# Kernel optimization log

Measured on AMD Instinct MI355X. Metric: run time of the kernel, lower is better.

## Reference

```python
import jax, jax.numpy as jnp
import numpy as np

B, T, E, H, O = 64, 512, 512, 512, 512

def setup_inputs() -> dict:
    key = jax.random.key(0)
    k1, k2, k3, k4, k5 = jax.random.split(key, 5)
    s1 = 1.0 / np.sqrt(E + H)
    s2 = 1.0 / np.sqrt(H)
    return {
        "x": jax.random.normal(k1, (B, T, E), dtype=jnp.float32),
        "W1": jax.random.uniform(k2, (H, E + H), dtype=jnp.float32, minval=-s1, maxval=s1),
        "b1": jax.random.uniform(k3, (H,), dtype=jnp.float32, minval=-s1, maxval=s1),
        "W2": jax.random.uniform(k4, (O, H), dtype=jnp.float32, minval=-s2, maxval=s2),
        "b2": jax.random.uniform(k5, (O,), dtype=jnp.float32, minval=-s2, maxval=s2),
    }

def reference(x, W1, b1, W2, b2):
    b = x.shape[0]
    h0 = jnp.zeros((b, x.shape[2]), dtype=x.dtype)

    def step(hidden, xt):
        inp = jnp.concatenate([xt, hidden], axis=1)          # [b, e+h]
        hidden = jax.nn.relu(inp @ W1.T + b1)                # [b, h]
        out = hidden @ W2.T + b2                             # [b, o]
        return hidden, out

    # scan over time: x -> [t, b, e]
    h_final, outs = jax.lax.scan(step, h0, jnp.swapaxes(x, 0, 1))
    return jnp.swapaxes(outs, 0, 1), h_final
```

## Files before the change

### kernel.cpp

```cpp
#include <hip/hip_runtime.h>
#include <cstddef>

#define T_STEPS 512
#define BATCH   64
#define EDIM    512
#define HDIM    512
#define ODIM    512

#define HPAD    520
#define HALF    256

typedef __bf16 bf16;
typedef __bf16 bf16x4 __attribute__((ext_vector_type(4)));
typedef __bf16 bf16x8 __attribute__((ext_vector_type(8)));
typedef float  f32x4  __attribute__((ext_vector_type(4)));

template <typename XT, bool REMAP>
__global__ __launch_bounds__(256) void gemm_mfma_kernel(
    const XT* __restrict__ X, int ldx,
    const float* __restrict__ W, int ldw, int kw0,
    const float* __restrict__ bias,
    float* __restrict__ C, int ldc, int K)
{
  __shared__ __align__(16) bf16 Asm[8 * 64 * 8];
  __shared__ __align__(16) bf16 Bsm[8 * 64 * 8];

  const int tid  = threadIdx.x;
  const int row0 = blockIdx.x * 128;
  const int col0 = blockIdx.y * 128;
  const int w    = tid >> 6, lane = tid & 63;
  const int q    = lane >> 4, nl = lane & 15;
  const int wm   = w >> 1, wn = w & 1;

  f32x4 acc[4][4] = {};

  for (int k0 = 0; k0 < K; k0 += 32) {
#pragma unroll
    for (int rep = 0; rep < 2; ++rep) {
      int idx = tid + rep * 256;
      int mt = idx >> 6, l2 = idx & 63;
      const XT* src = X + (size_t)(row0 + mt * 16 + (l2 & 15)) * ldx
                        + k0 + (l2 >> 4) * 8;
      bf16x8 v;
#pragma unroll
      for (int u = 0; u < 8; ++u) v[u] = (bf16)(float)src[u];
      *(bf16x8*)&Asm[(size_t)idx * 8] = v;
    }
#pragma unroll
    for (int rep = 0; rep < 2; ++rep) {
      int idx = tid + rep * 256;
      int nt = idx >> 6, l2 = idx & 63;
      const float* src = W + (size_t)(col0 + nt * 16 + (l2 & 15)) * ldw
                           + kw0 + k0 + (l2 >> 4) * 8;
      bf16x8 v;
#pragma unroll
      for (int u = 0; u < 8; ++u) v[u] = (bf16)src[u];
      *(bf16x8*)&Bsm[(size_t)idx * 8] = v;
    }
    __syncthreads();

    bf16x8 a[4], b[4];
#pragma unroll
    for (int i = 0; i < 4; ++i)
      a[i] = *(bf16x8*)&Asm[(size_t)((wm * 4 + i) * 64 + lane) * 8];
#pragma unroll
    for (int j = 0; j < 4; ++j)
      b[j] = *(bf16x8*)&Bsm[(size_t)((wn * 4 + j) * 64 + lane) * 8];
#pragma unroll
    for (int i = 0; i < 4; ++i)
#pragma unroll
      for (int j = 0; j < 4; ++j)
        acc[i][j] = __builtin_amdgcn_mfma_f32_16x16x32_bf16(a[i], b[j], acc[i][j], 0, 0, 0);
    __syncthreads();
  }

#pragma unroll
  for (int i = 0; i < 4; ++i)
#pragma unroll
    for (int j = 0; j < 4; ++j) {
      int colg = col0 + wn * 64 + j * 16 + nl;
#pragma unroll
      for (int r = 0; r < 4; ++r) {
        size_t rowg = (size_t)(row0 + wm * 64 + i * 16 + q * 4 + r);
        size_t crow = REMAP ? (((rowg & (T_STEPS - 1)) << 6) | (rowg >> 9)) : rowg;
        C[crow * ldc + colg] = acc[i][j][r] + bias[colg];
      }
    }
}

__global__ __launch_bounds__(512, 2) void scan_split_kernel(
    const float* __restrict__ A,
    const float* __restrict__ W1,
    bf16* __restrict__ Hbf,
    int* __restrict__ flags)
{
  const int bid = blockIdx.x;
  int c, s;
  if (bid < 4)                   { c = bid;     s = 0; }
  else if (bid >= 8 && bid < 12) { c = bid - 8; s = 1; }
  else return;

  __shared__ __align__(16) bf16 hsm[16 * HPAD];

  const int tid   = threadIdx.x;
  const int col0  = s * HALF;
  const int pcol0 = (1 - s) * HALF;
  const int rb0   = c * 16;
  const int w     = tid >> 6, lane = tid & 63;
  const int q     = lane >> 4, nl = lane & 15;
  const int n0    = col0 + w * 32;
  const int m_ex  = tid >> 5;
  const int j_ex  = tid & 31;

  int* myflag = flags + (c * 2 + s) * 32;
  int* paflag = flags + (c * 2 + (1 - s)) * 32;

  bf16x8 Wreg[2][16];
#pragma unroll
  for (int i = 0; i < 2; ++i) {
    const float* wrow = W1 + (size_t)(n0 + i * 16 + nl) * (EDIM + HDIM) + EDIM + q * 8;
#pragma unroll
    for (int j = 0; j < 16; ++j) {
      int kg = (j < 8) ? (s * 8 + j) : ((1 - s) * 8 + (j - 8));
      const float* src = wrow + kg * 32;
      bf16x8 v;
#pragma unroll
      for (int u = 0; u < 8; ++u) v[u] = (bf16)src[u];
      Wreg[i][j] = v;
    }
  }

  f32x4 An[2];
  {
    const float* ap = A + ((size_t)(rb0 + nl)) * HDIM + n0 + q * 4;
    An[0] = *(const f32x4*)ap;
    An[1] = *(const f32x4*)(ap + 16);
  }

  f32x4 acc[2];

  for (int t = 0; t < T_STEPS; ++t) {
    acc[0] = An[0];
    acc[1] = An[1];
    {
      int tn = (t + 1 < T_STEPS) ? t + 1 : 0;
      const float* ap = A + ((size_t)tn * BATCH + rb0 + nl) * HDIM + n0 + q * 4;
      An[0] = *(const f32x4*)ap;
      An[1] = *(const f32x4*)(ap + 16);
    }

    unsigned long long p0 = 0, p1 = 0;
    if (t > 0) {
      while (__hip_atomic_load(paflag, __ATOMIC_RELAXED,
                               __HIP_MEMORY_SCOPE_AGENT) < t) {}
      unsigned long long* src = (unsigned long long*)(
          Hbf + ((size_t)(rb0 + m_ex) * T_STEPS + (t - 1)) * HDIM + pcol0 + j_ex * 8);
      p0 = __hip_atomic_load(src,     __ATOMIC_RELAXED, __HIP_MEMORY_SCOPE_AGENT);
      p1 = __hip_atomic_load(src + 1, __ATOMIC_RELAXED, __HIP_MEMORY_SCOPE_AGENT);
    }

    if (t > 0) {
#pragma unroll
      for (int kk = 0; kk < 8; ++kk) {
        bf16x8 af = *(bf16x8*)&hsm[nl * HPAD + col0 + kk * 32 + q * 8];
        acc[0] = __builtin_amdgcn_mfma_f32_16x16x32_bf16(Wreg[0][kk], af, acc[0], 0, 0, 0);
        acc[1] = __builtin_amdgcn_mfma_f32_16x16x32_bf16(Wreg[1][kk], af, acc[1], 0, 0, 0);
      }
      {
        union { unsigned long long u[2]; bf16x8 v; } P;
        P.u[0] = p0; P.u[1] = p1;
        *(bf16x8*)&hsm[m_ex * HPAD + pcol0 + j_ex * 8] = P.v;
      }
      __syncthreads();
#pragma unroll
      for (int kk = 0; kk < 8; ++kk) {
        bf16x8 af = *(bf16x8*)&hsm[nl * HPAD + pcol0 + kk * 32 + q * 8];
        acc[0] = __builtin_amdgcn_mfma_f32_16x16x32_bf16(Wreg[0][8 + kk], af, acc[0], 0, 0, 0);
        acc[1] = __builtin_amdgcn_mfma_f32_16x16x32_bf16(Wreg[1][8 + kk], af, acc[1], 0, 0, 0);
      }
    }

#pragma unroll
    for (int i = 0; i < 2; ++i) {
      bf16x4 hv;
#pragma unroll
      for (int r = 0; r < 4; ++r) hv[r] = (bf16)fmaxf(acc[i][r], 0.0f);
      *(bf16x4*)&hsm[nl * HPAD + n0 + i * 16 + q * 4] = hv;
      *(bf16x4*)(Hbf + ((size_t)(rb0 + nl) * T_STEPS + t) * HDIM + n0 + i * 16 + q * 4) = hv;
    }

    __syncthreads();
    if (tid == 0) {
      __threadfence();
      __hip_atomic_fetch_add(myflag, 1, __ATOMIC_RELAXED,
                             __HIP_MEMORY_SCOPE_AGENT);
    }
  }
}

__global__ __launch_bounds__(256) void copy_hfinal_kernel(
    const bf16* __restrict__ Hbf, float* __restrict__ out)
{
  int i = blockIdx.x * blockDim.x + threadIdx.x;
  int b = i / HDIM, n = i % HDIM;
  out[i] = (float)Hbf[((size_t)b * T_STEPS + (T_STEPS - 1)) * HDIM + n];
}

extern "C" void kernel_launch(void* const* d_in, const int* in_sizes, int n_in,
                              void* d_out, int out_size, void* d_ws, size_t ws_size,
                              hipStream_t stream) {
  const float* x  = (const float*)d_in[0];
  const float* W1 = (const float*)d_in[1];
  const float* b1 = (const float*)d_in[2];
  const float* W2 = (const float*)d_in[3];
  const float* b2 = (const float*)d_in[4];

  float* out = (float*)d_out;
  float* A   = out;

  bf16* Hbf  = (bf16*)d_ws;
  int* flags = (int*)((char*)d_ws + (size_t)BATCH * T_STEPS * HDIM * 2);

  hipMemsetAsync(flags, 0, 8 * 32 * sizeof(int), stream);

  {
    dim3 grid(BATCH * T_STEPS / 128, HDIM / 128);
    gemm_mfma_kernel<float, true><<<grid, 256, 0, stream>>>(
        x, EDIM, W1, EDIM + HDIM, 0, b1, A, HDIM, EDIM);
  }

  scan_split_kernel<<<16, 512, 0, stream>>>(A, W1, Hbf, flags);

  {
    dim3 grid(BATCH * T_STEPS / 128, ODIM / 128);
    gemm_mfma_kernel<bf16, false><<<grid, 256, 0, stream>>>(
        Hbf, HDIM, W2, HDIM, 0, b2, out, ODIM, HDIM);
  }

  copy_hfinal_kernel<<<(BATCH * HDIM) / 256, 256, 0, stream>>>(
      Hbf, out + (size_t)BATCH * T_STEPS * ODIM);
}
```

Measured before the change: 1.574 ms.

## Run recurrent scan in one block per batch chunk, dropping cross-block flag sync

The recurrent scan now gives each 16-row batch chunk a single 512-thread block that computes all 512 hidden columns, rather than two blocks that swapped half-states through global memory and spin-waited on atomic flags every timestep. Because the full recurrent weight slice no longer fits in registers, a quarter of it is staged in LDS (about 128 KB of dynamic shared memory) and the rest stays in registers. The hidden-state write to global memory is deferred by one step so it overlaps with the next step's compute. This removes the per-step inter-block handshake latency, but each block now does twice the MFMA work per step and reads part of the weights from LDS.

```diff
diff --git a/kernel.cpp b/kernel.cpp
--- a/kernel.cpp
+++ b/kernel.cpp
@@ -8,7 +8,9 @@
 #define ODIM    512
 
 #define HPAD    520
-#define HALF    256
+#define W_ELEMS (32 * 4 * 64 * 8)
+#define H_ELEMS (16 * HPAD)
+#define SMEM_BYTES ((W_ELEMS + H_ELEMS) * 2)
 
 typedef __bf16 bf16;
 typedef __bf16 bf16x4 __attribute__((ext_vector_type(4)));
@@ -88,113 +90,125 @@
     }
 }
 
-__global__ __launch_bounds__(512, 2) void scan_split_kernel(
+__global__ __launch_bounds__(512, 2) void scan_big_kernel(
     const float* __restrict__ A,
     const float* __restrict__ W1,
-    bf16* __restrict__ Hbf,
-    int* __restrict__ flags)
+    bf16* __restrict__ Hbf)
 {
-  const int bid = blockIdx.x;
-  int c, s;
-  if (bid < 4)                   { c = bid;     s = 0; }
-  else if (bid >= 8 && bid < 12) { c = bid - 8; s = 1; }
-  else return;
-
-  __shared__ __align__(16) bf16 hsm[16 * HPAD];
-
-  const int tid   = threadIdx.x;
-  const int col0  = s * HALF;
-  const int pcol0 = (1 - s) * HALF;
-  const int rb0   = c * 16;
-  const int w     = tid >> 6, lane = tid & 63;
-  const int q     = lane >> 4, nl = lane & 15;
-  const int n0    = col0 + w * 32;
-  const int m_ex  = tid >> 5;
-  const int j_ex  = tid & 31;
-
-  int* myflag = flags + (c * 2 + s) * 32;
-  int* paflag = flags + (c * 2 + (1 - s)) * 32;
-
-  bf16x8 Wreg[2][16];
-#pragma unroll
-  for (int i = 0; i < 2; ++i) {
-    const float* wrow = W1 + (size_t)(n0 + i * 16 + nl) * (EDIM + HDIM) + EDIM + q * 8;
-#pragma unroll
-    for (int j = 0; j < 16; ++j) {
-      int kg = (j < 8) ? (s * 8 + j) : ((1 - s) * 8 + (j - 8));
-      const float* src = wrow + kg * 32;
+  extern __shared__ __align__(16) bf16 smem[];
+  bf16* Wlds = smem;
+  bf16* hsm  = smem + W_ELEMS;
+
+  const int tid  = threadIdx.x;
+  const int c    = blockIdx.x;
+  const int w    = tid >> 6, lane = tid & 63;
+  const int q    = lane >> 4, nl = lane & 15;
+  const int rb0  = c * 16;
+
+  for (int idx = tid; idx < 32 * 4 * 64; idx += 512) {
+    int l  = idx & 63;
+    int kt = (idx >> 6) & 3;
+    int tg = idx >> 8;
+    int n  = tg * 16 + (l & 15);
+    int k  = kt * 32 + (l >> 4) * 8;
+    const float* src = W1 + (size_t)n * (EDIM + HDIM) + EDIM + k;
+    bf16x8 v;
+#pragma unroll
+    for (int u = 0; u < 8; ++u) v[u] = (bf16)src[u];
+    *(bf16x8*)&Wlds[(size_t)idx * 8] = v;
+  }
+
+  bf16x8 Wreg[4][12];
+#pragma unroll
+  for (int i = 0; i < 4; ++i) {
+    int n = w * 64 + i * 16 + nl;
+    const float* wrow = W1 + (size_t)n * (EDIM + HDIM) + EDIM;
+#pragma unroll
+    for (int kt2 = 0; kt2 < 12; ++kt2) {
+      const float* src = wrow + (kt2 + 4) * 32 + q * 8;
       bf16x8 v;
 #pragma unroll
       for (int u = 0; u < 8; ++u) v[u] = (bf16)src[u];
-      Wreg[i][j] = v;
-    }
-  }
-
-  f32x4 An[2];
-  {
-    const float* ap = A + ((size_t)(rb0 + nl)) * HDIM + n0 + q * 4;
-    An[0] = *(const f32x4*)ap;
+      Wreg[i][kt2] = v;
+    }
+  }
+  __syncthreads();
+
+  f32x4 An[4];
+  {
+    const float* ap = A + (size_t)(rb0 + nl) * HDIM + w * 64 + q * 4;
+    An[0] = *(const f32x4*)(ap);
     An[1] = *(const f32x4*)(ap + 16);
-  }
-
-  f32x4 acc[2];
+    An[2] = *(const f32x4*)(ap + 32);
+    An[3] = *(const f32x4*)(ap + 48);
+  }
+
+  f32x4  acc[4];
+  bf16x4 hprev[4];
 
   for (int t = 0; t < T_STEPS; ++t) {
-    acc[0] = An[0];
-    acc[1] = An[1];
+    if (t > 0) {
+      bf16* dst = Hbf + ((size_t)(rb0 + nl) * T_STEPS + (t - 1)) * HDIM
+                  + w * 64 + q * 4;
+      *(bf16x4*)(dst)      = hprev[0];
+      *(bf16x4*)(dst + 16) = hprev[1];
+      *(bf16x4*)(dst + 32) = hprev[2];
+      *(bf16x4*)(dst + 48) = hprev[3];
+    }
+
+#pragma unroll
+    for (int i = 0; i < 4; ++i) acc[i] = An[i];
     {
       int tn = (t + 1 < T_STEPS) ? t + 1 : 0;
-      const float* ap = A + ((size_t)tn * BATCH + rb0 + nl) * HDIM + n0 + q * 4;
-      An[0] = *(const f32x4*)ap;
+      const float* ap = A + ((size_t)tn * BATCH + rb0 + nl) * HDIM + w * 64 + q * 4;
+      An[0] = *(const f32x4*)(ap);
       An[1] = *(const f32x4*)(ap + 16);
-    }
-
-    unsigned long long p0 = 0, p1 = 0;
+      An[2] = *(const f32x4*)(ap + 32);
+      An[3] = *(const f32x4*)(ap + 48);
+    }
+
     if (t > 0) {
-      while (__hip_atomic_load(paflag, __ATOMIC_RELAXED,
-                               __HIP_MEMORY_SCOPE_AGENT) < t) {}
-      unsigned long long* src = (unsigned long long*)(
-          Hbf + ((size_t)(rb0 + m_ex) * T_STEPS + (t - 1)) * HDIM + pcol0 + j_ex * 8);
-      p0 = __hip_atomic_load(src,     __ATOMIC_RELAXED, __HIP_MEMORY_SCOPE_AGENT);
-      p1 = __hip_atomic_load(src + 1, __ATOMIC_RELAXED, __HIP_MEMORY_SCOPE_AGENT);
-    }
-
-    if (t > 0) {
-#pragma unroll
-      for (int kk = 0; kk < 8; ++kk) {
-        bf16x8 af = *(bf16x8*)&hsm[nl * HPAD + col0 + kk * 32 + q * 8];
-        acc[0] = __builtin_amdgcn_mfma_f32_16x16x32_bf16(Wreg[0][kk], af, acc[0], 0, 0, 0);
-        acc[1] = __builtin_amdgcn_mfma_f32_16x16x32_bf16(Wreg[1][kk], af, acc[1], 0, 0, 0);
+#pragma unroll
+      for (int kt = 0; kt < 16; ++kt) {
+        bf16x8 af = *(bf16x8*)&hsm[nl * HPAD + kt * 32 + q * 8];
+        if (kt < 4) {
+#pragma unroll
+          for (int i = 0; i < 4; ++i) {
+            bf16x8 wb = *(bf16x8*)&Wlds[(size_t)(((w * 4 + i) * 4 + kt) * 64 + lane) * 8];
+            acc[i] = __builtin_amdgcn_mfma_f32_16x16x32_bf16(wb, af, acc[i], 0, 0, 0);
+          }
+        } else {
+#pragma unroll
+          for (int i = 0; i < 4; ++i)
+            acc[i] = __builtin_amdgcn_mfma_f32_16x16x32_bf16(Wreg[i][kt - 4], af, acc[i], 0, 0, 0);
+        }
       }
-      {
-        union { unsigned long long u[2]; bf16x8 v; } P;
-        P.u[0] = p0; P.u[1] = p1;
-        *(bf16x8*)&hsm[m_ex * HPAD + pcol0 + j_ex * 8] = P.v;
+    }
+
+    __syncthreads();
+
+#pragma unroll
+    for (int i = 0; i < 4; ++i) {
+      bf16x4 hv;
+#pragma unroll
+      for (int r = 0; r < 4; ++r) {
+        float v = acc[i][r] > 0.0f ? acc[i][r] : 0.0f;
+        hv[r] = (bf16)v;
       }
-      __syncthreads();
-#pragma unroll
-      for (int kk = 0; kk < 8; ++kk) {
-        bf16x8 af = *(bf16x8*)&hsm[nl * HPAD + pcol0 + kk * 32 + q * 8];
-        acc[0] = __builtin_amdgcn_mfma_f32_16x16x32_bf16(Wreg[0][8 + kk], af, acc[0], 0, 0, 0);
-        acc[1] = __builtin_amdgcn_mfma_f32_16x16x32_bf16(Wreg[1][8 + kk], af, acc[1], 0, 0, 0);
-      }
-    }
-
-#pragma unroll
-    for (int i = 0; i < 2; ++i) {
-      bf16x4 hv;
-#pragma unroll
-      for (int r = 0; r < 4; ++r) hv[r] = (bf16)fmaxf(acc[i][r], 0.0f);
-      *(bf16x4*)&hsm[nl * HPAD + n0 + i * 16 + q * 4] = hv;
-      *(bf16x4*)(Hbf + ((size_t)(rb0 + nl) * T_STEPS + t) * HDIM + n0 + i * 16 + q * 4) = hv;
-    }
-
-    __syncthreads();
-    if (tid == 0) {
-      __threadfence();
-      __hip_atomic_fetch_add(myflag, 1, __ATOMIC_RELAXED,
-                             __HIP_MEMORY_SCOPE_AGENT);
-    }
+      *(bf16x4*)&hsm[nl * HPAD + w * 64 + i * 16 + q * 4] = hv;
+      hprev[i] = hv;
+    }
+
+    __syncthreads();
+  }
+
+  {
+    bf16* dst = Hbf + ((size_t)(rb0 + nl) * T_STEPS + (T_STEPS - 1)) * HDIM
+                + w * 64 + q * 4;
+    *(bf16x4*)(dst)      = hprev[0];
+    *(bf16x4*)(dst + 16) = hprev[1];
+    *(bf16x4*)(dst + 32) = hprev[2];
+    *(bf16x4*)(dst + 48) = hprev[3];
   }
 }
 
@@ -219,9 +233,6 @@
   float* A   = out;
 
   bf16* Hbf  = (bf16*)d_ws;
-  int* flags = (int*)((char*)d_ws + (size_t)BATCH * T_STEPS * HDIM * 2);
-
-  hipMemsetAsync(flags, 0, 8 * 32 * sizeof(int), stream);
 
   {
     dim3 grid(BATCH * T_STEPS / 128, HDIM / 128);
@@ -229,7 +240,10 @@
         x, EDIM, W1, EDIM + HDIM, 0, b1, A, HDIM, EDIM);
   }
 
-  scan_split_kernel<<<16, 512, 0, stream>>>(A, W1, Hbf, flags);
+  hipFuncSetAttribute(
+      reinterpret_cast<const void*>(scan_big_kernel),
+      hipFuncAttributeMaxDynamicSharedMemorySize, SMEM_BYTES);
+  scan_big_kernel<<<4, 512, SMEM_BYTES, stream>>>(A, W1, Hbf);
 
   {
     dim3 grid(BATCH * T_STEPS / 128, ODIM / 128);
```

Measured after the change: 1.608 ms. 1.02x slower.

## Restructure scan exchange with compact double-buffered partner buffers and LDS-resident weights

Applied to the files above, without the earlier changes.

Moves the per-step hidden-state exchange between the paired scan blocks out of the large Hbf array and into small double-buffered exchange buffers. The partner's half is now read straight into registers and fed to the MFMAs, which removes one LDS round trip and one __syncthreads per step. Part of the recurrent weights now lives in LDS instead of registers to relieve register pressure, and the local hidden buffer is double-buffered with an XOR swizzle. The flag update becomes a plain store with s_sleep in the poll loop instead of a threadfence plus fetch_add. This risks memory-ordering problems, since the fence was removed and relaxed atomics are relied on for visibility.

```diff
diff --git a/kernel.cpp b/kernel.cpp
--- a/kernel.cpp
+++ b/kernel.cpp
@@ -6,9 +6,11 @@
 #define EDIM    512
 #define HDIM    512
 #define ODIM    512
-
-#define HPAD    520
 #define HALF    256
+
+#define WLDS_ELEMS (16 * 5 * 64 * 8)
+#define HB_ELEMS   (16 * HALF)
+#define SMEM_BYTES ((WLDS_ELEMS + 2 * HB_ELEMS) * 2)
 
 typedef __bf16 bf16;
 typedef __bf16 bf16x4 __attribute__((ext_vector_type(4)));
@@ -88,114 +90,179 @@
     }
 }
 
-__global__ __launch_bounds__(512, 2) void scan_split_kernel(
+template <int S>
+__device__ __forceinline__ void scan_half(
     const float* __restrict__ A,
     const float* __restrict__ W1,
     bf16* __restrict__ Hbf,
-    int* __restrict__ flags)
+    int* myflag, int* paflag,
+    bf16* __restrict__ mybuf,
+    const bf16* __restrict__ pbuf,
+    bf16* Wlds, bf16* h0, bf16* h1, int rb0)
 {
+  const int tid  = threadIdx.x;
+  const int w    = tid >> 6, lane = tid & 63;
+  const int q    = lane >> 4, nl = lane & 15;
+  const int col0 = S * HALF;
+  const int sw   = (nl & 7) << 3;
+  const int tg0  = w * 2;
+
+  for (int idx = tid; idx < 16 * 5 * 64; idx += 512) {
+    int l  = idx & 63;
+    int kt = (idx >> 6) % 5;
+    int tg = (idx >> 6) / 5;
+    int n  = col0 + tg * 16 + (l & 15);
+    int k  = kt * 32 + (l >> 4) * 8;
+    const float* src = W1 + (size_t)n * (EDIM + HDIM) + EDIM + k;
+    bf16x8 v;
+#pragma unroll
+    for (int u = 0; u < 8; ++u) v[u] = (bf16)src[u];
+    *(bf16x8*)&Wlds[(size_t)idx * 8] = v;
+  }
+
+  bf16x8 Wreg[2][11];
+#pragma unroll
+  for (int i = 0; i < 2; ++i) {
+    const float* wrow = W1 + (size_t)(col0 + w * 32 + i * 16 + nl) * (EDIM + HDIM)
+                        + EDIM + q * 8;
+#pragma unroll
+    for (int j = 0; j < 11; ++j) {
+      const float* src = wrow + (j + 5) * 32;
+      bf16x8 v;
+#pragma unroll
+      for (int u = 0; u < 8; ++u) v[u] = (bf16)src[u];
+      Wreg[i][j] = v;
+    }
+  }
+  __syncthreads();
+
+  f32x4 An[2];
+  {
+    const float* ap = A + (size_t)(rb0 + nl) * HDIM + col0 + w * 32 + q * 4;
+    An[0] = *(const f32x4*)ap;
+    An[1] = *(const f32x4*)(ap + 16);
+  }
+
+  f32x4 acc[2];
+  union PU { unsigned long long u[2]; bf16x8 v; };
+  union HB { bf16x4 v; unsigned long long u; };
+
+  for (int t = 0; t < T_STEPS; ++t) {
+    bf16* hr = (t & 1) ? h1 : h0;
+    bf16* hw = (t & 1) ? h0 : h1;
+
+    unsigned long long pl0[8], pl1[8];
+    if (t > 0) {
+      for (;;) {
+        int v = __hip_atomic_load(paflag, __ATOMIC_RELAXED,
+                                  __HIP_MEMORY_SCOPE_AGENT);
+        if (v >= t) break;
+        __builtin_amdgcn_s_sleep(1);
+      }
+      const bf16* pb = pbuf + ((t - 1) & 1) * HB_ELEMS;
+      unsigned long long* pr = (unsigned long long*)(pb + nl * HALF + q * 8);
+#pragma unroll
+      for (int j = 0; j < 8; ++j) {
+        pl0[j] = __hip_atomic_load(pr + j * 8,     __ATOMIC_RELAXED,
+                                   __HIP_MEMORY_SCOPE_AGENT);
+        pl1[j] = __hip_atomic_load(pr + j * 8 + 1, __ATOMIC_RELAXED,
+                                   __HIP_MEMORY_SCOPE_AGENT);
+      }
+    }
+
+    acc[0] = An[0];
+    acc[1] = An[1];
+    {
+      int tn = (t + 1 < T_STEPS) ? t + 1 : 0;
+      const float* ap = A + ((size_t)tn * BATCH + rb0 + nl) * HDIM
+                        + col0 + w * 32 + q * 4;
+      An[0] = *(const f32x4*)ap;
+      An[1] = *(const f32x4*)(ap + 16);
+    }
+
+    if (t > 0) {
+#pragma unroll
+      for (int j = 0; j < 8; ++j) {
+        bf16x8 af = *(bf16x8*)&hr[nl * HALF + ((j * 32 + q * 8) ^ sw)];
+        const int ktg = S * 8 + j;
+#pragma unroll
+        for (int i = 0; i < 2; ++i) {
+          bf16x8 wb;
+          if (ktg < 5)
+            wb = *(bf16x8*)&Wlds[(size_t)(((tg0 + i) * 5 + ktg) * 64 + lane) * 8];
+          else
+            wb = Wreg[i][ktg - 5];
+          acc[i] = __builtin_amdgcn_mfma_f32_16x16x32_bf16(wb, af, acc[i], 0, 0, 0);
+        }
+      }
+#pragma unroll
+      for (int j = 0; j < 8; ++j) {
+        PU pu; pu.u[0] = pl0[j]; pu.u[1] = pl1[j];
+        const int ktg = (1 - S) * 8 + j;
+#pragma unroll
+        for (int i = 0; i < 2; ++i) {
+          bf16x8 wb;
+          if (ktg < 5)
+            wb = *(bf16x8*)&Wlds[(size_t)(((tg0 + i) * 5 + ktg) * 64 + lane) * 8];
+          else
+            wb = Wreg[i][ktg - 5];
+          acc[i] = __builtin_amdgcn_mfma_f32_16x16x32_bf16(wb, pu.v, acc[i], 0, 0, 0);
+        }
+      }
+    }
+
+    {
+      bf16* mb = mybuf + (t & 1) * HB_ELEMS;
+#pragma unroll
+      for (int i = 0; i < 2; ++i) {
+        bf16x4 hv;
+#pragma unroll
+        for (int r = 0; r < 4; ++r)
+          hv[r] = (bf16)fmaxf(acc[i][r], 0.0f);
+        int colL = w * 32 + i * 16 + q * 4;
+        *(bf16x4*)&hw[nl * HALF + (colL ^ sw)] = hv;
+        HB hb; hb.v = hv;
+        __hip_atomic_store((unsigned long long*)(mb + nl * HALF + colL), hb.u,
+                           __ATOMIC_RELAXED, __HIP_MEMORY_SCOPE_AGENT);
+        *(bf16x4*)(Hbf + ((size_t)(rb0 + nl) * T_STEPS + t) * HDIM
+                   + col0 + colL) = hv;
+      }
+    }
+
+    __syncthreads();
+    if (tid == 0)
+      __hip_atomic_store(myflag, t + 1, __ATOMIC_RELAXED,
+                         __HIP_MEMORY_SCOPE_AGENT);
+  }
+}
+
+__global__ __launch_bounds__(512, 2) void scan_pair_kernel(
+    const float* __restrict__ A,
+    const float* __restrict__ W1,
+    bf16* __restrict__ Hbf,
+    int* __restrict__ flags,
+    bf16* __restrict__ exch)
+{
+  extern __shared__ __align__(16) bf16 smem[];
+  bf16* Wlds = smem;
+  bf16* h0   = smem + WLDS_ELEMS;
+  bf16* h1   = h0 + HB_ELEMS;
+
   const int bid = blockIdx.x;
   int c, s;
   if (bid < 4)                   { c = bid;     s = 0; }
   else if (bid >= 8 && bid < 12) { c = bid - 8; s = 1; }
   else return;
 
-  __shared__ __align__(16) bf16 hsm[16 * HPAD];
-
-  const int tid   = threadIdx.x;
-  const int col0  = s * HALF;
-  const int pcol0 = (1 - s) * HALF;
-  const int rb0   = c * 16;
-  const int w     = tid >> 6, lane = tid & 63;
-  const int q     = lane >> 4, nl = lane & 15;
-  const int n0    = col0 + w * 32;
-  const int m_ex  = tid >> 5;
-  const int j_ex  = tid & 31;
-
   int* myflag = flags + (c * 2 + s) * 32;
   int* paflag = flags + (c * 2 + (1 - s)) * 32;
-
-  bf16x8 Wreg[2][16];
-#pragma unroll
-  for (int i = 0; i < 2; ++i) {
-    const float* wrow = W1 + (size_t)(n0 + i * 16 + nl) * (EDIM + HDIM) + EDIM + q * 8;
-#pragma unroll
-    for (int j = 0; j < 16; ++j) {
-      int kg = (j < 8) ? (s * 8 + j) : ((1 - s) * 8 + (j - 8));
-      const float* src = wrow + kg * 32;
-      bf16x8 v;
-#pragma unroll
-      for (int u = 0; u < 8; ++u) v[u] = (bf16)src[u];
-      Wreg[i][j] = v;
-    }
-  }
-
-  f32x4 An[2];
-  {
-    const float* ap = A + ((size_t)(rb0 + nl)) * HDIM + n0 + q * 4;
-    An[0] = *(const f32x4*)ap;
-    An[1] = *(const f32x4*)(ap + 16);
-  }
-
-  f32x4 acc[2];
-
-  for (int t = 0; t < T_STEPS; ++t) {
-    acc[0] = An[0];
-    acc[1] = An[1];
-    {
-      int tn = (t + 1 < T_STEPS) ? t + 1 : 0;
-      const float* ap = A + ((size_t)tn * BATCH + rb0 + nl) * HDIM + n0 + q * 4;
-      An[0] = *(const f32x4*)ap;
-      An[1] = *(const f32x4*)(ap + 16);
-    }
-
-    unsigned long long p0 = 0, p1 = 0;
-    if (t > 0) {
-      while (__hip_atomic_load(paflag, __ATOMIC_RELAXED,
-                               __HIP_MEMORY_SCOPE_AGENT) < t) {}
-      unsigned long long* src = (unsigned long long*)(
-          Hbf + ((size_t)(rb0 + m_ex) * T_STEPS + (t - 1)) * HDIM + pcol0 + j_ex * 8);
-      p0 = __hip_atomic_load(src,     __ATOMIC_RELAXED, __HIP_MEMORY_SCOPE_AGENT);
-      p1 = __hip_atomic_load(src + 1, __ATOMIC_RELAXED, __HIP_MEMORY_SCOPE_AGENT);
-    }
-
-    if (t > 0) {
-#pragma unroll
-      for (int kk = 0; kk < 8; ++kk) {
-        bf16x8 af = *(bf16x8*)&hsm[nl * HPAD + col0 + kk * 32 + q * 8];
-        acc[0] = __builtin_amdgcn_mfma_f32_16x16x32_bf16(Wreg[0][kk], af, acc[0], 0, 0, 0);
-        acc[1] = __builtin_amdgcn_mfma_f32_16x16x32_bf16(Wreg[1][kk], af, acc[1], 0, 0, 0);
-      }
-      {
-        union { unsigned long long u[2]; bf16x8 v; } P;
-        P.u[0] = p0; P.u[1] = p1;
-        *(bf16x8*)&hsm[m_ex * HPAD + pcol0 + j_ex * 8] = P.v;
-      }
-      __syncthreads();
-#pragma unroll
-      for (int kk = 0; kk < 8; ++kk) {
-        bf16x8 af = *(bf16x8*)&hsm[nl * HPAD + pcol0 + kk * 32 + q * 8];
-        acc[0] = __builtin_amdgcn_mfma_f32_16x16x32_bf16(Wreg[0][8 + kk], af, acc[0], 0, 0, 0);
-        acc[1] = __builtin_amdgcn_mfma_f32_16x16x32_bf16(Wreg[1][8 + kk], af, acc[1], 0, 0, 0);
-      }
-    }
-
-#pragma unroll
-    for (int i = 0; i < 2; ++i) {
-      bf16x4 hv;
-#pragma unroll
-      for (int r = 0; r < 4; ++r) hv[r] = (bf16)fmaxf(acc[i][r], 0.0f);
-      *(bf16x4*)&hsm[nl * HPAD + n0 + i * 16 + q * 4] = hv;
-      *(bf16x4*)(Hbf + ((size_t)(rb0 + nl) * T_STEPS + t) * HDIM + n0 + i * 16 + q * 4) = hv;
-    }
-
-    __syncthreads();
-    if (tid == 0) {
-      __threadfence();
-      __hip_atomic_fetch_add(myflag, 1, __ATOMIC_RELAXED,
-                             __HIP_MEMORY_SCOPE_AGENT);
-    }
-  }
+  bf16* mybuf = exch + (size_t)((c * 2 + s) * 2) * HB_ELEMS;
+  bf16* pbuf  = exch + (size_t)((c * 2 + (1 - s)) * 2) * HB_ELEMS;
+
+  if (s == 0)
+    scan_half<0>(A, W1, Hbf, myflag, paflag, mybuf, pbuf, Wlds, h0, h1, c * 16);
+  else
+    scan_half<1>(A, W1, Hbf, myflag, paflag, mybuf, pbuf, Wlds, h0, h1, c * 16);
 }
 
 __global__ __launch_bounds__(256) void copy_hfinal_kernel(
@@ -219,9 +286,11 @@
   float* A   = out;
 
   bf16* Hbf  = (bf16*)d_ws;
-  int* flags = (int*)((char*)d_ws + (size_t)BATCH * T_STEPS * HDIM * 2);
-
-  hipMemsetAsync(flags, 0, 8 * 32 * sizeof(int), stream);
+  char* tail = (char*)d_ws + (size_t)BATCH * T_STEPS * HDIM * 2;
+  int*  flags = (int*)tail;
+  bf16* exch  = (bf16*)(tail + 4096);
+
+  hipMemsetAsync(flags, 0, 4096, stream);
 
   {
     dim3 grid(BATCH * T_STEPS / 128, HDIM / 128);
@@ -229,7 +298,10 @@
         x, EDIM, W1, EDIM + HDIM, 0, b1, A, HDIM, EDIM);
   }
 
-  scan_split_kernel<<<16, 512, 0, stream>>>(A, W1, Hbf, flags);
+  hipFuncSetAttribute(
+      reinterpret_cast<const void*>(scan_pair_kernel),
+      hipFuncAttributeMaxDynamicSharedMemorySize, SMEM_BYTES);
+  scan_pair_kernel<<<16, 512, SMEM_BYTES, stream>>>(A, W1, Hbf, flags, exch);
 
   {
     dim3 grid(BATCH * T_STEPS / 128, ODIM / 128);
```

Measured after the change: 3.106 ms. +97.3%, slower.
